# Kernel tuning notes

Measured on AMD Instinct MI355X. Metric: run time of the kernel, lower is better.

Reference implementation:

```python
import jax, jax.numpy as jnp
import numpy as np

B, F, S, H1, H2 = 4096, 512, 32, 64, 32


def setup_inputs() -> dict:
    key = jax.random.key(0)
    ks = jax.random.split(key, 9)
    x = jax.random.normal(ks[0], (B, F), dtype=jnp.float32)
    # ExU layer init: truncated_normal(mean=4, std=0.5) on weight, std=0.5 on bias
    W0 = 4.0 + 0.5 * jax.random.normal(ks[1], (F, S, S), dtype=jnp.float32)
    b0 = 0.5 * jax.random.normal(ks[2], (F, S), dtype=jnp.float32)
    # ReLU hidden layers: xavier-ish weights, small biases
    W1 = jax.random.normal(ks[3], (F, S, H1), dtype=jnp.float32) * np.sqrt(2.0 / (S + H1))
    b1 = 0.5 * jax.random.normal(ks[4], (F, S), dtype=jnp.float32)
    W2 = jax.random.normal(ks[5], (F, H1, H2), dtype=jnp.float32) * np.sqrt(2.0 / (H1 + H2))
    b2 = 0.5 * jax.random.normal(ks[6], (F, H1), dtype=jnp.float32)
    Wl = jax.random.normal(ks[7], (F, H2), dtype=jnp.float32) * np.sqrt(2.0 / (H2 + 1))
    out_bias = jnp.zeros((1,), dtype=jnp.float32)
    return {"x": x, "W0": W0, "b0": b0, "W1": W1, "b1": b1,
            "W2": W2, "b2": b2, "Wl": Wl, "out_bias": out_bias}


def reference(x, W0, b0, W1, b1, W2, b2, Wl, out_bias):
    # ExU shallow layer per feature: clip((x_f - b0_f) @ exp(W0_f), 0, 1)
    # x[:, :, None] - b0 broadcasts scalar feature to (B, F, S)
    h = jnp.clip(jnp.einsum('bfs,fsh->bfh', x[:, :, None] - b0[None], jnp.exp(W0)), 0.0, 1.0)
    # ReLU hidden layers: relu((h - b) @ W)
    h = jax.nn.relu(jnp.einsum('bfs,fsh->bfh', h - b1[None], W1))   # (B, F, H1)
    h = jax.nn.relu(jnp.einsum('bfh,fho->bfo', h - b2[None], W2))   # (B, F, H2)
    # per-feature Linear(H2 -> 1, no bias), concatenated over features
    f_out = jnp.einsum('bfo,fo->bf', h, Wl)                          # (B, F)
    # forward_type == 'sum' (feature_dropout is identity at inference)
    return f_out.sum(axis=-1) + out_bias[0], f_out
```

## Files before the change

### kernel.cpp

```cpp
#include <hip/hip_runtime.h>

typedef __attribute__((ext_vector_type(8))) short short8;
typedef __attribute__((ext_vector_type(4))) float f32x4;
typedef unsigned int uint32;

namespace {
constexpr int F = 512, NB = 4096;
constexpr int RPB = 2048;
constexpr size_t OFF_XT   = 0;
constexpr size_t OFF_FT   = OFF_XT + (size_t)F * NB * 4;
constexpr size_t OFF_PART = OFF_FT + (size_t)F * NB * 4;
constexpr size_t WS_NEED  = OFF_PART + (size_t)8 * NB * 4;
}

__device__ __forceinline__ uint32 cvtpk(float lo, float hi) {
    uint32 r;
    asm("v_cvt_pk_bf16_f32 %0, %1, %2" : "=v"(r) : "v"(lo), "v"(hi));
    return r;
}
__device__ __forceinline__ float clip01(float v) {
    return __builtin_amdgcn_fmed3f(v, 0.f, 1.f);
}

__global__ __launch_bounds__(256) void nam_xt(const float* __restrict__ x, char* ws) {
    __shared__ float tb[64][65];
    const int bb = blockIdx.x * 64, fb = blockIdx.y * 64;
    const int c = threadIdx.x & 63, r4 = threadIdx.x >> 6;
#pragma unroll
    for (int i = 0; i < 16; ++i) {
        int r = i * 4 + r4;
        tb[r][c] = x[(size_t)(bb + r) * F + fb + c];
    }
    __syncthreads();
    float* xT = (float*)(ws + OFF_XT);
#pragma unroll
    for (int i = 0; i < 16; ++i) {
        int fr = i * 4 + r4;
        xT[(size_t)(fb + fr) * NB + bb + c] = tb[c][fr];
    }
}

__global__ __launch_bounds__(256, 4) void nam_mfma(
    const float* __restrict__ W0, const float* __restrict__ b0,
    const float* __restrict__ W1, const float* __restrict__ b1,
    const float* __restrict__ W2, const float* __restrict__ b2,
    const float* __restrict__ Wl, char* __restrict__ ws)
{
    const int f = blockIdx.y;
    const int rbase = blockIdx.x * RPB;
    const int t = threadIdx.x;
    const int lane = t & 63, w = t >> 6;
    const int g = lane >> 4, rr = lane & 15;

    __shared__ float sx[RPB];
    __shared__ float pa[8][32], pc[8][32], pd2[8][32];
    __shared__ float pd1[4][64];
    __shared__ float sA[32], sC[32], sd1[64], sd2[32];

    const float* W0f = W0 + (size_t)f * 1024;
    const float* W1f = W1 + (size_t)f * 2048;
    const float* W2f = W2 + (size_t)f * 2048;

    {
        const float4* src = (const float4*)((const float*)(ws + OFF_XT) + (size_t)f * NB + rbase);
        float4* dst = (float4*)sx;
        dst[t] = src[t];
        dst[t + 256] = src[t + 256];
    }

    {
        int j = t & 31, sc = t >> 5;
        float a = 0.f, c = 0.f;
#pragma unroll
        for (int k = 0; k < 4; ++k) {
            int s = sc * 4 + k;
            float e = expf(W0f[s * 32 + j]);
            a += e; c += b0[f * 32 + s] * e;
        }
        pa[sc][j] = a; pc[sc][j] = c;
    }
    {
        int j = t & 63, sc = t >> 6;
        float d = 0.f;
#pragma unroll
        for (int k = 0; k < 8; ++k) {
            int s = sc * 8 + k;
            d += b1[f * 32 + s] * W1f[s * 64 + j];
        }
        pd1[sc][j] = d;
    }
    {
        int o = t & 31, hc = t >> 5;
        float d = 0.f;
#pragma unroll
        for (int k = 0; k < 8; ++k) {
            int h = hc * 8 + k;
            d += b2[f * 64 + h] * W2f[h * 32 + o];
        }
        pd2[hc][o] = d;
    }

    union U8 { uint32 u[4]; short8 s8; };
    short8 w1f[4], w2f[2][2];
#pragma unroll
    for (int mi = 0; mi < 4; ++mi) {
        int col = 32 * (mi & 1) + 8 * (rr >> 2) + 4 * (mi >> 1) + (rr & 3);
        const float* base = W1f + (size_t)(8 * g) * 64 + col;
        U8 v;
        v.u[0] = cvtpk(base[0],   base[64]);
        v.u[1] = cvtpk(base[128], base[192]);
        v.u[2] = cvtpk(base[256], base[320]);
        v.u[3] = cvtpk(base[384], base[448]);
        w1f[mi] = v.s8;
    }
#pragma unroll
    for (int m2 = 0; m2 < 2; ++m2)
#pragma unroll
        for (int kc = 0; kc < 2; ++kc) {
            const float* base = W2f + (size_t)(32 * kc + 8 * g) * 32 + 16 * m2 + rr;
            U8 v;
            v.u[0] = cvtpk(base[0],  base[32]);
            v.u[1] = cvtpk(base[64], base[96]);
            v.u[2] = cvtpk(base[128], base[160]);
            v.u[3] = cvtpk(base[192], base[224]);
            w2f[m2][kc] = v.s8;
        }

    __syncthreads();
    if (t < 32) {
        float a = 0.f, c = 0.f, d = 0.f;
#pragma unroll
        for (int k = 0; k < 8; ++k) { a += pa[k][t]; c += pc[k][t]; d += pd2[k][t]; }
        sA[t] = a; sC[t] = c; sd2[t] = d;
    } else if (t < 96) {
        int j = t - 32; float d = 0.f;
#pragma unroll
        for (int k = 0; k < 4; ++k) d += pd1[k][j];
        sd1[j] = d;
    }
    __syncthreads();

    float Aq[8], nCq[8];
#pragma unroll
    for (int q = 0; q < 8; ++q) { Aq[q] = sA[8 * g + q]; nCq[q] = -sC[8 * g + q]; }
    f32x4 nd1[4];
#pragma unroll
    for (int mi = 0; mi < 4; ++mi)
#pragma unroll
        for (int r = 0; r < 4; ++r)
            nd1[mi][r] = -sd1[32 * (mi & 1) + 8 * g + 4 * (mi >> 1) + r];
    f32x4 nd2[2];
#pragma unroll
    for (int m2 = 0; m2 < 2; ++m2)
#pragma unroll
        for (int r = 0; r < 4; ++r) nd2[m2][r] = -sd2[16 * m2 + 4 * g + r];
    float wlv[8];
#pragma unroll
    for (int m2 = 0; m2 < 2; ++m2)
#pragma unroll
        for (int r = 0; r < 4; ++r) wlv[m2 * 4 + r] = Wl[f * 32 + 16 * m2 + 4 * g + r];

    const float* sxw = sx + w * 512;
    float* outp = (float*)(ws + OFF_FT) + (size_t)f * NB + rbase + w * 512;

    for (int tile = 0; tile < 32; ++tile) {
        float xv = sxw[tile * 16 + rr];
        U8 hb;
        hb.u[0] = cvtpk(clip01(fmaf(xv, Aq[0], nCq[0])), clip01(fmaf(xv, Aq[1], nCq[1])));
        hb.u[1] = cvtpk(clip01(fmaf(xv, Aq[2], nCq[2])), clip01(fmaf(xv, Aq[3], nCq[3])));
        hb.u[2] = cvtpk(clip01(fmaf(xv, Aq[4], nCq[4])), clip01(fmaf(xv, Aq[5], nCq[5])));
        hb.u[3] = cvtpk(clip01(fmaf(xv, Aq[6], nCq[6])), clip01(fmaf(xv, Aq[7], nCq[7])));
        short8 b0f = hb.s8;

        f32x4 a0 = __builtin_amdgcn_mfma_f32_16x16x32_bf16(w1f[0], b0f, nd1[0], 0, 0, 0);
        f32x4 a1 = __builtin_amdgcn_mfma_f32_16x16x32_bf16(w1f[1], b0f, nd1[1], 0, 0, 0);
        f32x4 a2 = __builtin_amdgcn_mfma_f32_16x16x32_bf16(w1f[2], b0f, nd1[2], 0, 0, 0);
        f32x4 a3 = __builtin_amdgcn_mfma_f32_16x16x32_bf16(w1f[3], b0f, nd1[3], 0, 0, 0);

        U8 r0, r1;
        r0.u[0] = cvtpk(fmaxf(a0[0], 0.f), fmaxf(a0[1], 0.f));
        r0.u[1] = cvtpk(fmaxf(a0[2], 0.f), fmaxf(a0[3], 0.f));
        r0.u[2] = cvtpk(fmaxf(a2[0], 0.f), fmaxf(a2[1], 0.f));
        r0.u[3] = cvtpk(fmaxf(a2[2], 0.f), fmaxf(a2[3], 0.f));
        r1.u[0] = cvtpk(fmaxf(a1[0], 0.f), fmaxf(a1[1], 0.f));
        r1.u[1] = cvtpk(fmaxf(a1[2], 0.f), fmaxf(a1[3], 0.f));
        r1.u[2] = cvtpk(fmaxf(a3[0], 0.f), fmaxf(a3[1], 0.f));
        r1.u[3] = cvtpk(fmaxf(a3[2], 0.f), fmaxf(a3[3], 0.f));
        short8 b2f0 = r0.s8, b2f1 = r1.s8;

        f32x4 c0 = __builtin_amdgcn_mfma_f32_16x16x32_bf16(w2f[0][0], b2f0, nd2[0], 0, 0, 0);
        c0 = __builtin_amdgcn_mfma_f32_16x16x32_bf16(w2f[0][1], b2f1, c0, 0, 0, 0);
        f32x4 c1 = __builtin_amdgcn_mfma_f32_16x16x32_bf16(w2f[1][0], b2f0, nd2[1], 0, 0, 0);
        c1 = __builtin_amdgcn_mfma_f32_16x16x32_bf16(w2f[1][1], b2f1, c1, 0, 0, 0);

        float p0 = 0.f, p1 = 0.f;
#pragma unroll
        for (int r = 0; r < 4; ++r) {
            p0 = fmaf(fmaxf(c0[r], 0.f), wlv[r], p0);
            p1 = fmaf(fmaxf(c1[r], 0.f), wlv[4 + r], p1);
        }
        float p = p0 + p1;
        p += __shfl_xor(p, 16, 64);
        p += __shfl_xor(p, 32, 64);
        if (lane < 16) outp[tile * 16 + lane] = p;
    }
}

__global__ __launch_bounds__(256) void nam_post(const char* ws, float* __restrict__ fout,
                                                float* __restrict__ part) {
    __shared__ float tb[64][65];
    __shared__ float ps[4][64];
    const int bb = blockIdx.x * 64, fb = blockIdx.y * 64;
    const int c = threadIdx.x & 63, r4 = threadIdx.x >> 6;
    const float* foutT = (const float*)(ws + OFF_FT);
    float s = 0.f;
#pragma unroll
    for (int i = 0; i < 16; ++i) {
        int fr = i * 4 + r4;
        float v = foutT[(size_t)(fb + fr) * NB + bb + c];
        tb[fr][c] = v;
        s += v;
    }
    ps[r4][c] = s;
    __syncthreads();
#pragma unroll
    for (int i = 0; i < 16; ++i) {
        int br = i * 4 + r4;
        fout[(size_t)(bb + br) * F + fb + c] = tb[c][br];
    }
    if (threadIdx.x < 64)
        part[(size_t)blockIdx.y * NB + bb + threadIdx.x] =
            ps[0][threadIdx.x] + ps[1][threadIdx.x] + ps[2][threadIdx.x] + ps[3][threadIdx.x];
}

__global__ __launch_bounds__(256) void nam_sum(const float* __restrict__ part,
                                               const float* __restrict__ ob,
                                               float* __restrict__ out0) {
    int r = blockIdx.x * 256 + threadIdx.x;
    float s = ob[0];
#pragma unroll
    for (int k = 0; k < 8; ++k) s += part[(size_t)k * NB + r];
    out0[r] = s;
}

namespace fbk {
constexpr int S = 32, H1 = 64, H2 = 32, BLK = 256, ROWS = 2, P1 = 36;
}
__global__ __launch_bounds__(256, 2) void fb_main(
    const float* __restrict__ x,  const float* __restrict__ W0,
    const float* __restrict__ b0, const float* __restrict__ W1,
    const float* __restrict__ b1, const float* __restrict__ W2,
    const float* __restrict__ b2, const float* __restrict__ Wl,
    float* __restrict__ fout) {
    using namespace fbk;
    const int f = blockIdx.y;
    const int bbase = blockIdx.x * (BLK * ROWS);
    const int t = threadIdx.x;
    __shared__ float W0e[S * S];
    __shared__ float W1t[H1 * P1];
    __shared__ float W2l[H1 * H2];
    __shared__ float sb0[S], sb1[S], sb2[H1];
    __shared__ float sA[S], sC[S], sd1[H1], sd2[H2], sWl[H2];
    {
        float4 wv = *reinterpret_cast<const float4*>(W0 + (size_t)f * S * S + t * 4);
        W0e[t * 4 + 0] = expf(wv.x); W0e[t * 4 + 1] = expf(wv.y);
        W0e[t * 4 + 2] = expf(wv.z); W0e[t * 4 + 3] = expf(wv.w);
    }
    if (t < S) sb0[t] = b0[f * S + t];
    else if (t < 2 * S) sb1[t - S] = b1[f * S + (t - S)];
    else if (t < 2 * S + H1) sb2[t - 2 * S] = b2[f * H1 + (t - 2 * S)];
    else if (t < 2 * S + H1 + H2) sWl[t - 2 * S - H1] = Wl[f * H2 + (t - 2 * S - H1)];
#pragma unroll
    for (int k = 0; k < (S * H1) / BLK; ++k) {
        int i = t + BLK * k; int s = i >> 6, j = i & 63;
        W1t[j * P1 + s] = W1[(size_t)f * S * H1 + i];
    }
#pragma unroll
    for (int k = 0; k < (H1 * H2) / BLK; ++k) {
        int i = t + BLK * k; W2l[i] = W2[(size_t)f * H1 * H2 + i];
    }
    __syncthreads();
    if (t < S) {
        int j = t; float a = 0.f, c = 0.f;
#pragma unroll
        for (int s = 0; s < S; ++s) { float e = W0e[s * S + j]; a += e; c += sb0[s] * e; }
        sA[j] = a; sC[j] = c;
    } else if (t >= 64 && t < 64 + H1) {
        int j = t - 64; float d = 0.f;
#pragma unroll
        for (int s = 0; s < S; ++s) d += sb1[s] * W1t[j * P1 + s];
        sd1[j] = d;
    } else if (t >= 128 && t < 128 + H2) {
        int o = t - 128; float d = 0.f;
#pragma unroll
        for (int h = 0; h < H1; ++h) d += sb2[h] * W2l[h * H2 + o];
        sd2[o] = d;
    }
    __syncthreads();
    const int ra = bbase + t, rb = bbase + BLK + t;
    const float xa = x[(size_t)ra * F + f], xb = x[(size_t)rb * F + f];
    float h0a[S], h0b[S];
#pragma unroll
    for (int j = 0; j < S; ++j) {
        float A = sA[j], C = sC[j];
        h0a[j] = fminf(fmaxf(fmaf(xa, A, -C), 0.f), 1.f);
        h0b[j] = fminf(fmaxf(fmaf(xb, A, -C), 0.f), 1.f);
    }
    float acc2a[H2], acc2b[H2];
#pragma unroll
    for (int o = 0; o < H2; ++o) { float d = sd2[o]; acc2a[o] = -d; acc2b[o] = -d; }
#pragma unroll 2
    for (int j = 0; j < H1; ++j) {
        float wr[S];
#pragma unroll
        for (int q = 0; q < S / 4; ++q)
            *reinterpret_cast<float4*>(&wr[4 * q]) = reinterpret_cast<const float4*>(&W1t[j * P1])[q];
        float d1j = sd1[j];
        float pa0 = -d1j, pa1 = 0.f, pb0 = -d1j, pb1 = 0.f;
#pragma unroll
        for (int s = 0; s < S; s += 2) {
            pa0 = fmaf(h0a[s], wr[s], pa0); pb0 = fmaf(h0b[s], wr[s], pb0);
            pa1 = fmaf(h0a[s + 1], wr[s + 1], pa1); pb1 = fmaf(h0b[s + 1], wr[s + 1], pb1);
        }
        float h1a = fmaxf(pa0 + pa1, 0.f), h1b = fmaxf(pb0 + pb1, 0.f);
        float w2r[H2];
#pragma unroll
        for (int q = 0; q < H2 / 4; ++q)
            *reinterpret_cast<float4*>(&w2r[4 * q]) = reinterpret_cast<const float4*>(&W2l[j * H2])[q];
#pragma unroll
        for (int o = 0; o < H2; ++o) {
            acc2a[o] = fmaf(h1a, w2r[o], acc2a[o]); acc2b[o] = fmaf(h1b, w2r[o], acc2b[o]);
        }
    }
    float outa = 0.f, outb = 0.f;
#pragma unroll
    for (int o = 0; o < H2; ++o) {
        outa = fmaf(fmaxf(acc2a[o], 0.f), sWl[o], outa);
        outb = fmaf(fmaxf(acc2b[o], 0.f), sWl[o], outb);
    }
    fout[(size_t)ra * F + f] = outa;
    fout[(size_t)rb * F + f] = outb;
}
__global__ __launch_bounds__(256) void fb_rowsum(
    const float* __restrict__ fout, const float* __restrict__ out_bias,
    float* __restrict__ out0) {
    const int wave = threadIdx.x >> 6, lane = threadIdx.x & 63;
    const int b = blockIdx.x * 4 + wave;
    float s = 0.f;
#pragma unroll
    for (int k = 0; k < F / 64; ++k) s += fout[(size_t)b * F + k * 64 + lane];
#pragma unroll
    for (int off = 32; off; off >>= 1) s += __shfl_down(s, off, 64);
    if (lane == 0) out0[b] = s + out_bias[0];
}

extern "C" void kernel_launch(void* const* d_in, const int* in_sizes, int n_in,
                              void* d_out, int out_size, void* d_ws, size_t ws_size,
                              hipStream_t stream) {
    const float* x  = (const float*)d_in[0];
    const float* W0 = (const float*)d_in[1];
    const float* b0 = (const float*)d_in[2];
    const float* W1 = (const float*)d_in[3];
    const float* b1 = (const float*)d_in[4];
    const float* W2 = (const float*)d_in[5];
    const float* b2 = (const float*)d_in[6];
    const float* Wl = (const float*)d_in[7];
    const float* ob = (const float*)d_in[8];

    float* out0 = (float*)d_out;
    float* fout = out0 + NB;

    if (ws_size >= WS_NEED) {
        char* ws = (char*)d_ws;
        nam_xt  <<<dim3(NB / 64, F / 64), 256, 0, stream>>>(x, ws);
        nam_mfma<<<dim3(NB / RPB, F), 256, 0, stream>>>(W0, b0, W1, b1, W2, b2, Wl, ws);
        nam_post<<<dim3(NB / 64, F / 64), 256, 0, stream>>>(ws, fout, (float*)(ws + OFF_PART));
        nam_sum <<<NB / 256, 256, 0, stream>>>((const float*)(ws + OFF_PART), ob, out0);
    } else {
        dim3 grid(NB / (fbk::BLK * fbk::ROWS), F);
        fb_main<<<grid, fbk::BLK, 0, stream>>>(x, W0, b0, W1, b1, W2, b2, Wl, fout);
        fb_rowsum<<<NB / 4, 256, 0, stream>>>(fout, ob, out0);
    }
}
```

Measured before the change: 49.18 us.

## Fuse transposes into main MFMA kernel and precompute per-feature weight fragments

Replaces the four-kernel pipeline (x transpose, per-feature MFMA, output transpose+partial sum, final sum) with three kernels. A prep kernel converts each feature's W1/W2 into bf16 MFMA fragment images and precomputes the folded bias constants once in workspace. The main kernel uses 1024-thread blocks covering 16 features by 512 rows, staging x and outputs through padded shared memory so the global transposes and their intermediate round trips disappear. The cost is a larger block with heavier shared memory use (about 68 KB) and more partial sums for the final reduction.

```diff
diff --git a/kernel.cpp b/kernel.cpp
--- a/kernel.cpp
+++ b/kernel.cpp
@@ -6,11 +6,14 @@
 
 namespace {
 constexpr int F = 512, NB = 4096;
-constexpr int RPB = 2048;
-constexpr size_t OFF_XT   = 0;
-constexpr size_t OFF_FT   = OFF_XT + (size_t)F * NB * 4;
-constexpr size_t OFF_PART = OFF_FT + (size_t)F * NB * 4;
-constexpr size_t WS_NEED  = OFF_PART + (size_t)8 * NB * 4;
+constexpr int FB = 16;
+constexpr int RB = 512;
+constexpr int NFG = F / FB;
+constexpr size_t OFF_W1F  = 0;
+constexpr size_t OFF_W2F  = OFF_W1F + (size_t)F * 4 * 64 * 16;
+constexpr size_t OFF_ACD  = OFF_W2F + (size_t)F * 4 * 64 * 16;
+constexpr size_t OFF_PART = OFF_ACD + (size_t)F * 160 * 4;
+constexpr size_t WS_NEED  = OFF_PART + (size_t)NFG * NB * 4;
 }
 
 __device__ __forceinline__ uint32 cvtpk(float lo, float hi) {
@@ -22,86 +25,46 @@
     return __builtin_amdgcn_fmed3f(v, 0.f, 1.f);
 }
 
-__global__ __launch_bounds__(256) void nam_xt(const float* __restrict__ x, char* ws) {
-    __shared__ float tb[64][65];
-    const int bb = blockIdx.x * 64, fb = blockIdx.y * 64;
-    const int c = threadIdx.x & 63, r4 = threadIdx.x >> 6;
-#pragma unroll
-    for (int i = 0; i < 16; ++i) {
-        int r = i * 4 + r4;
-        tb[r][c] = x[(size_t)(bb + r) * F + fb + c];
-    }
-    __syncthreads();
-    float* xT = (float*)(ws + OFF_XT);
-#pragma unroll
-    for (int i = 0; i < 16; ++i) {
-        int fr = i * 4 + r4;
-        xT[(size_t)(fb + fr) * NB + bb + c] = tb[c][fr];
-    }
-}
-
-__global__ __launch_bounds__(256, 4) void nam_mfma(
+__global__ __launch_bounds__(256) void nam_prep(
     const float* __restrict__ W0, const float* __restrict__ b0,
     const float* __restrict__ W1, const float* __restrict__ b1,
     const float* __restrict__ W2, const float* __restrict__ b2,
-    const float* __restrict__ Wl, char* __restrict__ ws)
+    char* __restrict__ ws)
 {
-    const int f = blockIdx.y;
-    const int rbase = blockIdx.x * RPB;
     const int t = threadIdx.x;
-    const int lane = t & 63, w = t >> 6;
-    const int g = lane >> 4, rr = lane & 15;
-
-    __shared__ float sx[RPB];
-    __shared__ float pa[8][32], pc[8][32], pd2[8][32];
-    __shared__ float pd1[4][64];
-    __shared__ float sA[32], sC[32], sd1[64], sd2[32];
+    const int f = blockIdx.x * 4 + (t >> 6);
+    const int lane = t & 63, g = lane >> 4, rr = lane & 15;
 
     const float* W0f = W0 + (size_t)f * 1024;
     const float* W1f = W1 + (size_t)f * 2048;
     const float* W2f = W2 + (size_t)f * 2048;
-
+    float* acd = (float*)(ws + OFF_ACD) + (size_t)f * 160;
+
+    if (lane < 32) {
+        float a = 0.f, c = 0.f;
+#pragma unroll 4
+        for (int s = 0; s < 32; ++s) {
+            float e = expf(W0f[s * 32 + lane]);
+            a += e; c += b0[f * 32 + s] * e;
+        }
+        acd[lane] = a; acd[32 + lane] = c;
+    }
     {
-        const float4* src = (const float4*)((const float*)(ws + OFF_XT) + (size_t)f * NB + rbase);
-        float4* dst = (float4*)sx;
-        dst[t] = src[t];
-        dst[t + 256] = src[t + 256];
-    }
-
-    {
-        int j = t & 31, sc = t >> 5;
-        float a = 0.f, c = 0.f;
-#pragma unroll
-        for (int k = 0; k < 4; ++k) {
-            int s = sc * 4 + k;
-            float e = expf(W0f[s * 32 + j]);
-            a += e; c += b0[f * 32 + s] * e;
-        }
-        pa[sc][j] = a; pc[sc][j] = c;
-    }
-    {
-        int j = t & 63, sc = t >> 6;
         float d = 0.f;
-#pragma unroll
-        for (int k = 0; k < 8; ++k) {
-            int s = sc * 8 + k;
-            d += b1[f * 32 + s] * W1f[s * 64 + j];
-        }
-        pd1[sc][j] = d;
-    }
-    {
-        int o = t & 31, hc = t >> 5;
+#pragma unroll 4
+        for (int s = 0; s < 32; ++s) d += b1[f * 32 + s] * W1f[s * 64 + lane];
+        acd[64 + lane] = d;
+    }
+    if (lane < 32) {
         float d = 0.f;
-#pragma unroll
-        for (int k = 0; k < 8; ++k) {
-            int h = hc * 8 + k;
-            d += b2[f * 64 + h] * W2f[h * 32 + o];
-        }
-        pd2[hc][o] = d;
+#pragma unroll 4
+        for (int h = 0; h < 64; ++h) d += b2[f * 64 + h] * W2f[h * 32 + lane];
+        acd[128 + lane] = d;
     }
 
     union U8 { uint32 u[4]; short8 s8; };
-    short8 w1f[4], w2f[2][2];
+    short8* w1img = (short8*)(ws + OFF_W1F);
+    short8* w2img = (short8*)(ws + OFF_W2F);
 #pragma unroll
     for (int mi = 0; mi < 4; ++mi) {
         int col = 32 * (mi & 1) + 8 * (rr >> 2) + 4 * (mi >> 1) + (rr & 3);
@@ -111,7 +74,7 @@
         v.u[1] = cvtpk(base[128], base[192]);
         v.u[2] = cvtpk(base[256], base[320]);
         v.u[3] = cvtpk(base[384], base[448]);
-        w1f[mi] = v.s8;
+        w1img[((size_t)f * 4 + mi) * 64 + lane] = v.s8;
     }
 #pragma unroll
     for (int m2 = 0; m2 < 2; ++m2)
@@ -119,52 +82,73 @@
         for (int kc = 0; kc < 2; ++kc) {
             const float* base = W2f + (size_t)(32 * kc + 8 * g) * 32 + 16 * m2 + rr;
             U8 v;
-            v.u[0] = cvtpk(base[0],  base[32]);
-            v.u[1] = cvtpk(base[64], base[96]);
+            v.u[0] = cvtpk(base[0],   base[32]);
+            v.u[1] = cvtpk(base[64],  base[96]);
             v.u[2] = cvtpk(base[128], base[160]);
             v.u[3] = cvtpk(base[192], base[224]);
-            w2f[m2][kc] = v.s8;
-        }
+            w2img[((size_t)f * 4 + m2 * 2 + kc) * 64 + lane] = v.s8;
+        }
+}
+
+__global__ __launch_bounds__(1024, 4) void nam_main(
+    const float* __restrict__ x, const float* __restrict__ Wl,
+    char* __restrict__ ws, float* __restrict__ fout, float* __restrict__ part)
+{
+    const int fg = blockIdx.y;
+    const int f0 = fg * FB;
+    const int rbase = blockIdx.x * RB;
+    const int t = threadIdx.x;
+    const int w = t >> 6, lane = t & 63;
+    const int g = lane >> 4, rr = lane & 15;
+    const int f = f0 + w;
+
+    __shared__ float sx[RB * 17];
+    __shared__ float sfo[RB * 17];
+
+#pragma unroll
+    for (int k = 0; k < 8; ++k) {
+        int idx = t + 1024 * k;
+        int r = idx >> 4, fi = idx & 15;
+        sx[r * 17 + fi] = x[(size_t)(rbase + r) * F + f0 + fi];
+    }
+
+    const short8* w1img = (const short8*)(ws + OFF_W1F);
+    const short8* w2img = (const short8*)(ws + OFF_W2F);
+    short8 w1f[4], w2f[2][2];
+#pragma unroll
+    for (int mi = 0; mi < 4; ++mi) w1f[mi] = w1img[((size_t)f * 4 + mi) * 64 + lane];
+#pragma unroll
+    for (int m2 = 0; m2 < 2; ++m2)
+#pragma unroll
+        for (int kc = 0; kc < 2; ++kc)
+            w2f[m2][kc] = w2img[((size_t)f * 4 + m2 * 2 + kc) * 64 + lane];
+
+    const float* acd = (const float*)(ws + OFF_ACD) + (size_t)f * 160;
+    float Aq[8], nCq[8];
+#pragma unroll
+    for (int q = 0; q < 8; ++q) { Aq[q] = acd[8 * g + q]; nCq[q] = -acd[32 + 8 * g + q]; }
+    f32x4 nd1[4];
+#pragma unroll
+    for (int mi = 0; mi < 4; ++mi)
+#pragma unroll
+        for (int r = 0; r < 4; ++r)
+            nd1[mi][r] = -acd[64 + 32 * (mi & 1) + 8 * g + 4 * (mi >> 1) + r];
+    f32x4 nd2[2];
+#pragma unroll
+    for (int m2 = 0; m2 < 2; ++m2)
+#pragma unroll
+        for (int r = 0; r < 4; ++r) nd2[m2][r] = -acd[128 + 16 * m2 + 4 * g + r];
+    float wlv[8];
+#pragma unroll
+    for (int m2 = 0; m2 < 2; ++m2)
+#pragma unroll
+        for (int r = 0; r < 4; ++r) wlv[m2 * 4 + r] = Wl[f * 32 + 16 * m2 + 4 * g + r];
 
     __syncthreads();
-    if (t < 32) {
-        float a = 0.f, c = 0.f, d = 0.f;
-#pragma unroll
-        for (int k = 0; k < 8; ++k) { a += pa[k][t]; c += pc[k][t]; d += pd2[k][t]; }
-        sA[t] = a; sC[t] = c; sd2[t] = d;
-    } else if (t < 96) {
-        int j = t - 32; float d = 0.f;
-#pragma unroll
-        for (int k = 0; k < 4; ++k) d += pd1[k][j];
-        sd1[j] = d;
-    }
-    __syncthreads();
-
-    float Aq[8], nCq[8];
-#pragma unroll
-    for (int q = 0; q < 8; ++q) { Aq[q] = sA[8 * g + q]; nCq[q] = -sC[8 * g + q]; }
-    f32x4 nd1[4];
-#pragma unroll
-    for (int mi = 0; mi < 4; ++mi)
-#pragma unroll
-        for (int r = 0; r < 4; ++r)
-            nd1[mi][r] = -sd1[32 * (mi & 1) + 8 * g + 4 * (mi >> 1) + r];
-    f32x4 nd2[2];
-#pragma unroll
-    for (int m2 = 0; m2 < 2; ++m2)
-#pragma unroll
-        for (int r = 0; r < 4; ++r) nd2[m2][r] = -sd2[16 * m2 + 4 * g + r];
-    float wlv[8];
-#pragma unroll
-    for (int m2 = 0; m2 < 2; ++m2)
-#pragma unroll
-        for (int r = 0; r < 4; ++r) wlv[m2 * 4 + r] = Wl[f * 32 + 16 * m2 + 4 * g + r];
-
-    const float* sxw = sx + w * 512;
-    float* outp = (float*)(ws + OFF_FT) + (size_t)f * NB + rbase + w * 512;
-
+
+    union U8 { uint32 u[4]; short8 s8; };
     for (int tile = 0; tile < 32; ++tile) {
-        float xv = sxw[tile * 16 + rr];
+        float xv = sx[(tile * 16 + rr) * 17 + w];
         U8 hb;
         hb.u[0] = cvtpk(clip01(fmaf(xv, Aq[0], nCq[0])), clip01(fmaf(xv, Aq[1], nCq[1])));
         hb.u[1] = cvtpk(clip01(fmaf(xv, Aq[2], nCq[2])), clip01(fmaf(xv, Aq[3], nCq[3])));
@@ -202,35 +186,23 @@
         float p = p0 + p1;
         p += __shfl_xor(p, 16, 64);
         p += __shfl_xor(p, 32, 64);
-        if (lane < 16) outp[tile * 16 + lane] = p;
-    }
-}
-
-__global__ __launch_bounds__(256) void nam_post(const char* ws, float* __restrict__ fout,
-                                                float* __restrict__ part) {
-    __shared__ float tb[64][65];
-    __shared__ float ps[4][64];
-    const int bb = blockIdx.x * 64, fb = blockIdx.y * 64;
-    const int c = threadIdx.x & 63, r4 = threadIdx.x >> 6;
-    const float* foutT = (const float*)(ws + OFF_FT);
-    float s = 0.f;
-#pragma unroll
-    for (int i = 0; i < 16; ++i) {
-        int fr = i * 4 + r4;
-        float v = foutT[(size_t)(fb + fr) * NB + bb + c];
-        tb[fr][c] = v;
-        s += v;
-    }
-    ps[r4][c] = s;
+        if (lane < 16) sfo[(tile * 16 + lane) * 17 + w] = p;
+    }
+
     __syncthreads();
-#pragma unroll
-    for (int i = 0; i < 16; ++i) {
-        int br = i * 4 + r4;
-        fout[(size_t)(bb + br) * F + fb + c] = tb[c][br];
-    }
-    if (threadIdx.x < 64)
-        part[(size_t)blockIdx.y * NB + bb + threadIdx.x] =
-            ps[0][threadIdx.x] + ps[1][threadIdx.x] + ps[2][threadIdx.x] + ps[3][threadIdx.x];
+
+#pragma unroll
+    for (int k = 0; k < 8; ++k) {
+        int idx = t + 1024 * k;
+        int r = idx >> 4, fi = idx & 15;
+        float v = sfo[r * 17 + fi];
+        fout[(size_t)(rbase + r) * F + f0 + fi] = v;
+        v += __shfl_xor(v, 1, 64);
+        v += __shfl_xor(v, 2, 64);
+        v += __shfl_xor(v, 4, 64);
+        v += __shfl_xor(v, 8, 64);
+        if ((lane & 15) == 0) part[(size_t)fg * NB + rbase + r] = v;
+    }
 }
 
 __global__ __launch_bounds__(256) void nam_sum(const float* __restrict__ part,
@@ -239,13 +211,11 @@
     int r = blockIdx.x * 256 + threadIdx.x;
     float s = ob[0];
 #pragma unroll
-    for (int k = 0; k < 8; ++k) s += part[(size_t)k * NB + r];
+    for (int k = 0; k < NFG; ++k) s += part[(size_t)k * NB + r];
     out0[r] = s;
 }
 
-namespace fbk {
-constexpr int S = 32, H1 = 64, H2 = 32, BLK = 256, ROWS = 2, P1 = 36;
-}
+namespace fbk { constexpr int S = 32, H1 = 64, H2 = 32, BLK = 256, ROWS = 2, P1 = 36; }
 __global__ __launch_bounds__(256, 2) void fb_main(
     const float* __restrict__ x,  const float* __restrict__ W0,
     const float* __restrict__ b0, const float* __restrict__ W1,
@@ -372,10 +342,10 @@
 
     if (ws_size >= WS_NEED) {
         char* ws = (char*)d_ws;
-        nam_xt  <<<dim3(NB / 64, F / 64), 256, 0, stream>>>(x, ws);
-        nam_mfma<<<dim3(NB / RPB, F), 256, 0, stream>>>(W0, b0, W1, b1, W2, b2, Wl, ws);
-        nam_post<<<dim3(NB / 64, F / 64), 256, 0, stream>>>(ws, fout, (float*)(ws + OFF_PART));
-        nam_sum <<<NB / 256, 256, 0, stream>>>((const float*)(ws + OFF_PART), ob, out0);
+        float* part = (float*)(ws + OFF_PART);
+        nam_prep<<<F / 4, 256, 0, stream>>>(W0, b0, W1, b1, W2, b2, ws);
+        nam_main<<<dim3(NB / RB, NFG), 1024, 0, stream>>>(x, Wl, ws, fout, part);
+        nam_sum <<<NB / 256, 256, 0, stream>>>(part, ob, out0);
     } else {
         dim3 grid(NB / (fbk::BLK * fbk::ROWS), F);
         fb_main<<<grid, fbk::BLK, 0, stream>>>(x, W0, b0, W1, b1, W2, b2, Wl, fout);
```

Measured after the change: 58.34 us. 1.19x slower.
